# Kernel tuning notes

Measured on AMD Instinct MI355X. Metric: run time of the kernel, lower is better.

Reference implementation:

```python
import jax, jax.numpy as jnp
import numpy as np

B, N, CI, CO = 2, 64, 32, 32  # batch, n points, Rs_in channels (j), Rs_out channels (i)


def setup_inputs() -> dict:
    key = jax.random.key(0)
    kf, kg, kw = jax.random.split(key, 3)
    features = jax.random.normal(kf, (B, N, N, CI), dtype=jnp.float32)
    geometry = jax.random.normal(kg, (B, N, 3), dtype=jnp.float32)
    # Continuous kernel parameters: linear map from relative vector (xyz) to 6*CO*CI kernel entries
    W = jax.random.normal(kw, (3, 6 * CO * CI), dtype=jnp.float32) / jnp.sqrt(3.0)
    return {"features": features, "geometry": geometry, "W": W, "n_norm": 1}


def reference(features, geometry, W, n_norm):
    z, n = geometry.shape[:2]
    ci = features.shape[-1]
    co = W.shape[1] // (6 * ci)
    # rel[z, a, b] = r_b - r_a  (rb = unsqueeze(1), ra = unsqueeze(2))
    rel = geometry[:, None, :, :] - geometry[:, :, None, :]  # [z, a, b, 3]
    k = jnp.einsum('zabx,xk->zabk', rel, W).reshape(z, n, n, 6 * co, ci)
    k = k / jnp.sqrt(6.0 * (n_norm ** 2))
    k1, k2, k3, k4, k5, k6 = jnp.split(k, 6, axis=3)  # each [z, a, b, i, j]
    # Precompute shared feature reductions over c and d once (fused HBM savings)
    fs = features.sum(axis=2)   # sum over d -> [z, c, j]
    fd = features.sum(axis=1)   # sum over c -> [z, d, j]
    ft = fs.sum(axis=1)         # sum over c,d -> [z, j]
    out = jnp.einsum('zabij,zj->zabi', k1, ft)
    out = out + jnp.einsum('zacij,zcj->zai', k2, fs)[:, :, None, :]
    out = out + jnp.einsum('zadij,zdj->zai', k3, fd)[:, :, None, :]
    out = out + jnp.einsum('zbcij,zcj->zbi', k4, fs)[:, None, :, :]
    out = out + jnp.einsum('zbdij,zdj->zbi', k5, fd)[:, None, :, :]
    out = out + jnp.einsum('zcdij,zcdj->zi', k6, features)[:, None, None, :]
    return out  # [z, a, b, i]
```

## Files before the change

### kernel.cpp

```cpp
#include <hip/hip_runtime.h>
#include <math.h>

#define NZ 2
#define NN 64
#define NCI 32
#define NCO 32
#define NBZ 32

__device__ __forceinline__ void ld4(const float* __restrict__ p, float* d) {
    const float4 v = *(const float4*)p;
    d[0] = v.x; d[1] = v.y; d[2] = v.z; d[3] = v.w;
}

__global__ __launch_bounds__(1024) void k_single(const float* __restrict__ feat,
                                                 const float* __restrict__ geom,
                                                 const float* __restrict__ W,
                                                 const int* __restrict__ nnp,
                                                 float* __restrict__ out) {
    const int bid  = blockIdx.x;
    const int z    = bid >> 5;
    const int s    = bid & 31;
    const int tid  = threadIdx.x;
    const int lane = tid & 63;
    const int wv   = tid >> 6;

    __shared__ float gsh[NN * 3];
    __shared__ float wred[16][7][32];
    __shared__ float sacc[7][32];
    __shared__ float gred[3][32];
    __shared__ float stab[224];

    if (tid < NN * 3) gsh[tid] = geom[z * NN * 3 + tid];
    __syncthreads();

    const int cg = tid & 7;
    const int dh = (tid >> 3) & 1;
    const int c  = tid >> 4;
    const float gc0 = gsh[c * 3 + 0], gc1 = gsh[c * 3 + 1], gc2 = gsh[c * 3 + 2];

    float rs[4] = {0.f, 0.f, 0.f, 0.f};
    float Gd[3][4] = {{0.f}};
    const float* rowp = feat + ((size_t)z * 4096 + c * 64 + dh * 32) * NCI + cg * 4;
    #pragma unroll 8
    for (int t = 0; t < 32; ++t) {
        float f[4];
        ld4(rowp + t * NCI, f);
        const int d = dh * 32 + t;
        const float gd0 = gsh[d * 3 + 0], gd1 = gsh[d * 3 + 1], gd2 = gsh[d * 3 + 2];
        #pragma unroll
        for (int k = 0; k < 4; ++k) {
            rs[k] += f[k];
            Gd[0][k] = fmaf(gd0, f[k], Gd[0][k]);
            Gd[1][k] = fmaf(gd1, f[k], Gd[1][k]);
            Gd[2][k] = fmaf(gd2, f[k], Gd[2][k]);
        }
    }

    float v[7][4];
    #pragma unroll
    for (int k = 0; k < 4; ++k) {
        v[0][k] = rs[k];
        v[1][k] = gc0 * rs[k]; v[2][k] = gc1 * rs[k]; v[3][k] = gc2 * rs[k];
        v[4][k] = Gd[0][k];    v[5][k] = Gd[1][k];    v[6][k] = Gd[2][k];
    }
    #pragma unroll
    for (int q = 0; q < 7; ++q)
        #pragma unroll
        for (int k = 0; k < 4; ++k) {
            float t = v[q][k];
            t += __shfl_xor(t, 8);
            t += __shfl_xor(t, 16);
            t += __shfl_xor(t, 32);
            v[q][k] = t;
        }
    if (lane < 8) {
        #pragma unroll
        for (int q = 0; q < 7; ++q)
            #pragma unroll
            for (int k = 0; k < 4; ++k) wred[wv][q][lane * 4 + k] = v[q][k];
    }
    __syncthreads();
    if (tid < 224) {
        const int q = tid >> 5, j = tid & 31;
        float sum = 0.f;
        #pragma unroll
        for (int g = 0; g < 16; ++g) sum += wred[g][q][j];
        sacc[q][j] = sum;
    }
    __syncthreads();

    const int vn = *nnp;
    const float nnv = (vn > 0 && vn < (1 << 23)) ? (float)vn : __int_as_float(vn);
    const float scale = 1.0f / sqrtf(6.0f * nnv * nnv);

    if (tid < 768) {
        const int x = tid >> 8, i = (tid >> 3) & 31, jg = tid & 7;
        const float* Wp = W + x * 6 * NCO * NCI + i * NCI + jg * 4;
        float w[6][4];
        #pragma unroll
        for (int m = 0; m < 6; ++m) ld4(Wp + m * 1024, w[m]);
        float q1 = 0.f, q23 = 0.f, q45 = 0.f, gp = 0.f;
        #pragma unroll
        for (int k = 0; k < 4; ++k) {
            const int j = jg * 4 + k;
            const float ftj = sacc[0][j];
            const float gsj = sacc[1 + x][j];
            const float gdj = sacc[4 + x][j];
            q1  = fmaf(w[0][k], ftj, q1);
            q23 = fmaf(w[1][k] + w[2][k], ftj, q23);
            q45 = fmaf(w[3][k] + w[4][k], ftj, q45);
            gp  = fmaf(w[1][k] + w[3][k] - w[5][k], gsj, gp);
            gp  = fmaf(w[2][k] + w[4][k] + w[5][k], gdj, gp);
        }
        #pragma unroll
        for (int m = 1; m <= 4; m <<= 1) {
            q1  += __shfl_xor(q1, m);
            q23 += __shfl_xor(q23, m);
            q45 += __shfl_xor(q45, m);
            gp  += __shfl_xor(gp, m);
        }
        if (jg == 0) {
            stab[x * 32 + i]      = scale * (q1 + q23);
            stab[96 + x * 32 + i] = scale * (q1 - q45);
            gred[x][i] = gp;
        }
    }
    __syncthreads();
    if (tid < 32) stab[192 + tid] = scale * (gred[0][tid] + gred[1][tid] + gred[2][tid]);
    __syncthreads();

    const int r  = tid >> 3;
    const int ab = s * 128 + r;
    const int a = ab >> 6, b = ab & 63;
    const int i0 = cg * 4;
    float o4[4];
    #pragma unroll
    for (int k = 0; k < 4; ++k) o4[k] = stab[192 + i0 + k];
    #pragma unroll
    for (int x = 0; x < 3; ++x) {
        const float gb = gsh[b * 3 + x], ga = gsh[a * 3 + x];
        #pragma unroll
        for (int k = 0; k < 4; ++k)
            o4[k] = fmaf(gb, stab[96 + x * 32 + i0 + k],
                         fmaf(-ga, stab[x * 32 + i0 + k], o4[k]));
    }
    float4 o; o.x = o4[0]; o.y = o4[1]; o.z = o4[2]; o.w = o4[3];
    *(float4*)(out + ((size_t)(z * 4096 + ab)) * NCI + i0) = o;
}

extern "C" void kernel_launch(void* const* d_in, const int* in_sizes, int n_in,
                              void* d_out, int out_size, void* d_ws, size_t ws_size,
                              hipStream_t stream) {
    const float* feat = (const float*)d_in[0];
    const float* geom = (const float*)d_in[1];
    const float* W    = (const float*)d_in[2];
    const int*   nnp  = (const int*)d_in[3];

    k_single<<<NZ * NBZ, 1024, 0, stream>>>(feat, geom, W, nnp, (float*)d_out);
}
```

Baseline: 14.36 us.

## Split redundant per-block feature reduction into partial-sum and output kernels

```diff
diff --git a/kernel.cpp b/kernel.cpp
--- a/kernel.cpp
+++ b/kernel.cpp
@@ -5,63 +5,50 @@
 #define NN 64
 #define NCI 32
 #define NCO 32
-#define NBZ 32
+#define SLICES 32
 
 __device__ __forceinline__ void ld4(const float* __restrict__ p, float* d) {
     const float4 v = *(const float4*)p;
     d[0] = v.x; d[1] = v.y; d[2] = v.z; d[3] = v.w;
 }
 
-__global__ __launch_bounds__(1024) void k_single(const float* __restrict__ feat,
-                                                 const float* __restrict__ geom,
-                                                 const float* __restrict__ W,
-                                                 const int* __restrict__ nnp,
-                                                 float* __restrict__ out) {
+
+__global__ __launch_bounds__(1024) void k_part(const float* __restrict__ feat,
+                                               const float* __restrict__ geom,
+                                               const float* __restrict__ W,
+                                               const int* __restrict__ nnp,
+                                               float* __restrict__ part) {
     const int bid  = blockIdx.x;
     const int z    = bid >> 5;
     const int s    = bid & 31;
     const int tid  = threadIdx.x;
     const int lane = tid & 63;
     const int wv   = tid >> 6;
+    const int cg   = tid & 7;
+    const int pr   = tid >> 3;
 
     __shared__ float gsh[NN * 3];
     __shared__ float wred[16][7][32];
     __shared__ float sacc[7][32];
     __shared__ float gred[3][32];
-    __shared__ float stab[224];
 
     if (tid < NN * 3) gsh[tid] = geom[z * NN * 3 + tid];
     __syncthreads();
 
-    const int cg = tid & 7;
-    const int dh = (tid >> 3) & 1;
-    const int c  = tid >> 4;
-    const float gc0 = gsh[c * 3 + 0], gc1 = gsh[c * 3 + 1], gc2 = gsh[c * 3 + 2];
-
-    float rs[4] = {0.f, 0.f, 0.f, 0.f};
-    float Gd[3][4] = {{0.f}};
-    const float* rowp = feat + ((size_t)z * 4096 + c * 64 + dh * 32) * NCI + cg * 4;
-    #pragma unroll 8
-    for (int t = 0; t < 32; ++t) {
-        float f[4];
-        ld4(rowp + t * NCI, f);
-        const int d = dh * 32 + t;
-        const float gd0 = gsh[d * 3 + 0], gd1 = gsh[d * 3 + 1], gd2 = gsh[d * 3 + 2];
-        #pragma unroll
-        for (int k = 0; k < 4; ++k) {
-            rs[k] += f[k];
-            Gd[0][k] = fmaf(gd0, f[k], Gd[0][k]);
-            Gd[1][k] = fmaf(gd1, f[k], Gd[1][k]);
-            Gd[2][k] = fmaf(gd2, f[k], Gd[2][k]);
-        }
-    }
+    const int p = s * 128 + pr;
+    const int c = p >> 6, d = p & 63;
+    float f[4];
+    ld4(feat + ((size_t)z * 4096 + p) * NCI + cg * 4, f);
 
     float v[7][4];
     #pragma unroll
     for (int k = 0; k < 4; ++k) {
-        v[0][k] = rs[k];
-        v[1][k] = gc0 * rs[k]; v[2][k] = gc1 * rs[k]; v[3][k] = gc2 * rs[k];
-        v[4][k] = Gd[0][k];    v[5][k] = Gd[1][k];    v[6][k] = Gd[2][k];
+        v[0][k] = f[k];
+        #pragma unroll
+        for (int x = 0; x < 3; ++x) {
+            v[1 + x][k] = gsh[c * 3 + x] * f[k];
+            v[4 + x][k] = gsh[d * 3 + x] * f[k];
+        }
     }
     #pragma unroll
     for (int q = 0; q < 7; ++q)
@@ -93,6 +80,7 @@
     const float nnv = (vn > 0 && vn < (1 << 23)) ? (float)vn : __int_as_float(vn);
     const float scale = 1.0f / sqrtf(6.0f * nnv * nnv);
 
+    float* slot = part + (size_t)bid * 224;
     if (tid < 768) {
         const int x = tid >> 8, i = (tid >> 3) & 31, jg = tid & 7;
         const float* Wp = W + x * 6 * NCO * NCI + i * NCI + jg * 4;
@@ -120,19 +108,47 @@
             gp  += __shfl_xor(gp, m);
         }
         if (jg == 0) {
-            stab[x * 32 + i]      = scale * (q1 + q23);
-            stab[96 + x * 32 + i] = scale * (q1 - q45);
+            slot[x * 32 + i]      = scale * (q1 + q23);
+            slot[96 + x * 32 + i] = scale * (q1 - q45);
             gred[x][i] = gp;
         }
     }
     __syncthreads();
-    if (tid < 32) stab[192 + tid] = scale * (gred[0][tid] + gred[1][tid] + gred[2][tid]);
+    if (tid < 32)
+        slot[192 + tid] = scale * (gred[0][tid] + gred[1][tid] + gred[2][tid]);
+}
+
+__global__ __launch_bounds__(1024) void k_out(const float* __restrict__ part,
+                                              const float* __restrict__ geom,
+                                              float* __restrict__ out) {
+    const int bid = blockIdx.x;
+    const int z   = bid >> 5;
+    const int s   = bid & 31;
+    const int tid = threadIdx.x;
+
+    __shared__ float gsh[NN * 3];
+    __shared__ float red4[4][224];
+    __shared__ float stab[224];
+
+    if (tid < NN * 3) gsh[tid] = geom[z * NN * 3 + tid];
+
+    if (tid < 896) {
+        const int e = tid >> 2, sg = tid & 3;
+        const float* pz = part + ((size_t)z * 32 + sg * 8) * 224 + e;
+        float sum = 0.f;
+        #pragma unroll
+        for (int t = 0; t < 8; ++t) sum += pz[t * 224];
+        red4[sg][e] = sum;
+    }
+    __syncthreads();
+    if (tid < 224)
+        stab[tid] = red4[0][tid] + red4[1][tid] + red4[2][tid] + red4[3][tid];
     __syncthreads();
 
+    const int cg = tid & 7, i0 = cg * 4;
     const int r  = tid >> 3;
     const int ab = s * 128 + r;
     const int a = ab >> 6, b = ab & 63;
-    const int i0 = cg * 4;
     float o4[4];
     #pragma unroll
     for (int k = 0; k < 4; ++k) o4[k] = stab[192 + i0 + k];
@@ -156,5 +172,8 @@
     const float* W    = (const float*)d_in[2];
     const int*   nnp  = (const int*)d_in[3];
 
-    k_single<<<NZ * NBZ, 1024, 0, stream>>>(feat, geom, W, nnp, (float*)d_out);
+    float* part = (float*)d_ws;
+
+    k_part<<<NZ * SLICES, 1024, 0, stream>>>(feat, geom, W, nnp, part);
+    k_out<<<NZ * SLICES, 1024, 0, stream>>>(part, geom, (float*)d_out);
 }
```

After: 14.93 us. 4.0% more time.
